# Optimization experiments

Hardware: AMD Instinct MI355X
Metric: run time of the kernel (lower is better)

Reference implementation:

```python
import jax, jax.numpy as jnp
import numpy as np

V, H, L, T, B, S = 32000, 1024, 2, 64, 32, 64


def setup_inputs() -> dict:
    key = jax.random.key(0)
    ks = jax.random.split(key, 10)
    sc = 0.02
    return {
        "tokens": jax.random.randint(ks[0], (T, B), 0, V),
        "h0": jax.random.normal(ks[1], (L, B, H), jnp.float32) * sc,
        "c0": jax.random.normal(ks[2], (L, B, H), jnp.float32) * sc,
        "contexts": jax.random.normal(ks[3], (B, S, H), jnp.float32) * sc,
        "emb": jax.random.normal(ks[4], (V, H), jnp.float32) * sc,
        "W_ih": jax.random.normal(ks[5], (L, 4 * H, H), jnp.float32) * sc,
        "W_hh": jax.random.normal(ks[6], (L, 4 * H, H), jnp.float32) * sc,
        "b_ih": jnp.zeros((L, 4 * H), jnp.float32),
        "b_hh": jnp.zeros((L, 4 * H), jnp.float32),
        "W_in": jax.random.normal(ks[7], (H, H), jnp.float32) * sc,
        "b_in": jnp.zeros((H,), jnp.float32),
        "W_out": jax.random.normal(ks[8], (H, 2 * H), jnp.float32) * sc,
        "b_out": jnp.zeros((H,), jnp.float32),
    }


def _lstm_cell(x, h, c, Wih, Whh, bih, bhh):
    # PyTorch LSTMCell gate order: i, f, g, o
    gates = x @ Wih.T + bih + h @ Whh.T + bhh  # [B, 4H]
    i, f, g, o = jnp.split(gates, 4, axis=-1)
    c1 = jax.nn.sigmoid(f) * c + jax.nn.sigmoid(i) * jnp.tanh(g)
    h1 = jax.nn.sigmoid(o) * jnp.tanh(c1)
    return h1, c1


def reference(tokens, h0, c0, contexts, emb, W_ih, W_hh, b_ih, b_hh,
              W_in, b_in, W_out, b_out):
    # dropout is identity in eval mode
    embs = emb[tokens]  # [T, B, H]
    n_layers = h0.shape[0]

    def step(carry, x):
        h, c = carry
        hs, cs = [], []
        inp = x
        for l in range(n_layers):
            h1, c1 = _lstm_cell(inp, h[l], c[l], W_ih[l], W_hh[l], b_ih[l], b_hh[l])
            inp = h1
            hs.append(h1)
            cs.append(c1)
        # global (Luong general) attention
        gamma = inp @ W_in.T + b_in                      # [B, H]
        scores = jnp.einsum("bsh,bh->bs", contexts, gamma)
        w = jax.nn.softmax(scores, axis=-1)              # [B, S]
        ctx = jnp.einsum("bs,bsh->bh", w, contexts)      # [B, H]
        out = jnp.tanh(jnp.concatenate([ctx, inp], axis=-1) @ W_out.T + b_out)
        return (jnp.stack(hs), jnp.stack(cs)), (out, w)

    (hT, cT), (outputs, attns) = jax.lax.scan(step, (h0, c0), embs)
    return outputs, hT, cT  # outputs: [T, B, H]
```

## Files before the change

### kernel.cpp

```cpp
#include <hip/hip_runtime.h>
#include <hip/hip_bf16.h>

#define HDIM 1024
#define BDIM 32
#define TDIM 64
#define SDIM 64
#define NBLK 256

typedef __attribute__((ext_vector_type(8))) short short8;
typedef __attribute__((ext_vector_type(4))) short s4v;
typedef __attribute__((ext_vector_type(4))) float f32x4;
typedef unsigned short ushort;
typedef unsigned int uint;

__device__ __forceinline__ float sigm(float x){ return 1.f/(1.f+expf(-x)); }
__device__ __forceinline__ ushort f2bf(float x){
  uint u = __float_as_uint(x);
  u = (u + 0x7FFF + ((u>>16)&1)) >> 16;
  return (ushort)u;
}
#define MFMA16(a,b,c) __builtin_amdgcn_mfma_f32_16x16x32_bf16((a),(b),(c),0,0,0)
#define ALD(p)     __hip_atomic_load((p), __ATOMIC_RELAXED, __HIP_MEMORY_SCOPE_AGENT)
#define AST(p,v)   __hip_atomic_store((p),(v), __ATOMIC_RELAXED, __HIP_MEMORY_SCOPE_AGENT)

__device__ __forceinline__ void load8(const char* b, s4v* r){
  asm volatile(
    "global_load_dwordx2 %0, %8, off\n\t"
    "global_load_dwordx2 %1, %8, off offset:128\n\t"
    "global_load_dwordx2 %2, %8, off offset:256\n\t"
    "global_load_dwordx2 %3, %8, off offset:384\n\t"
    "global_load_dwordx2 %4, %8, off offset:2048\n\t"
    "global_load_dwordx2 %5, %8, off offset:2176\n\t"
    "global_load_dwordx2 %6, %8, off offset:2304\n\t"
    "global_load_dwordx2 %7, %8, off offset:2432\n\t"
    : "=&v"(r[0]), "=&v"(r[1]), "=&v"(r[2]), "=&v"(r[3]),
      "=&v"(r[4]), "=&v"(r[5]), "=&v"(r[6]), "=&v"(r[7])
    : "v"(b) : "memory");
}


__global__ void init_state_kernel(const float* __restrict__ h0,
                                  ushort* __restrict__ h0h,
                                  ushort* __restrict__ h1h){
  int i = blockIdx.x*256 + threadIdx.x;
  int l = i >> 15, r = i & 32767;
  int b = r >> 10, h = r & 1023;
  ushort* dst = l ? h1h : h0h;
  dst[(h>>2)*128 + b*4 + (h&3)] = f2bf(h0[i]);
}

__global__ void bar_init_kernel(int* flags){
  for(int i=threadIdx.x; i<1024; i+=256) flags[i] = 0;
}

__global__ void cast_kernel(const float* __restrict__ src, ushort* __restrict__ dst, int n4){
  int i = blockIdx.x*256 + threadIdx.x;
  if(i < n4){
    float4 v = ((const float4*)src)[i];
    ushort4 o; o.x=f2bf(v.x); o.y=f2bf(v.y); o.z=f2bf(v.z); o.w=f2bf(v.w);
    ((ushort4*)dst)[i] = o;
  }
}

__global__ void transpose_ctx_kernel(const float* __restrict__ ctx, ushort* __restrict__ ctxT){
  int b = blockIdx.y;
  int n = blockIdx.x*64 + (threadIdx.x & 63);
  int s0 = (threadIdx.x >> 6) * 16;
  for(int s=s0; s<s0+16; s++){
    float v = ctx[((size_t)b*SDIM + s)*HDIM + n];
    ctxT[((size_t)b*HDIM + n)*SDIM + s] = f2bf(v);
  }
}

__global__ void bias_kernel(const float* __restrict__ b_ih, const float* __restrict__ b_hh,
                            float* __restrict__ bias0, float* __restrict__ bias1){
  int i = blockIdx.x*256 + threadIdx.x;
  bias0[i] = b_ih[i] + b_hh[i];
  bias1[i] = b_ih[4096+i] + b_hh[4096+i];
}

__global__ void embed_kernel(const int* __restrict__ tokens,
                             const float* __restrict__ emb,
                             ushort* __restrict__ Xb){
  int tb = blockIdx.x;
  int tok = tokens[tb];
  const float4* src = (const float4*)(emb + (size_t)tok*HDIM);
  ushort4* dst = (ushort4*)(Xb + (size_t)tb*HDIM);
  float4 v = src[threadIdx.x];
  ushort4 o; o.x=f2bf(v.x); o.y=f2bf(v.y); o.z=f2bf(v.z); o.w=f2bf(v.w);
  dst[threadIdx.x] = o;
}

__global__ __launch_bounds__(256) void gemm_mfma_bt(
    const ushort* __restrict__ A0, const ushort* __restrict__ A1, int lda, int KSPLIT,
    const ushort* __restrict__ B, int ldb,
    const float* __restrict__ bias,
    float* __restrict__ C, int ldc, int K, int act){
  __shared__ ushort As[64][40];
  __shared__ ushort Bs[64][40];
  const int bm = blockIdx.y*64, bn = blockIdx.x*64;
  const int tid = threadIdx.x, w = tid>>6, lane = tid&63;
  const int quad = lane>>4, l16 = lane&15;
  const int mh = (w>>1)*32, nh = (w&1)*32;
  const int arow = tid>>2, aseg = (tid&3)*8;
  f32x4 acc[2][2];
  #pragma unroll
  for(int i=0;i<2;i++)
    #pragma unroll
    for(int j=0;j<2;j++) acc[i][j] = (f32x4){0.f,0.f,0.f,0.f};

  for(int k0=0;k0<K;k0+=32){
    int gk = k0 + aseg;
    const ushort* ap = (gk < KSPLIT) ? (A0 + (size_t)(bm+arow)*lda + gk)
                                     : (A1 + (size_t)(bm+arow)*lda + (gk - KSPLIT));
    *(float4*)&As[arow][aseg] = *(const float4*)ap;
    *(float4*)&Bs[arow][aseg] = *(const float4*)(B + (size_t)(bn+arow)*ldb + k0 + aseg);
    __syncthreads();
    short8 a0 = *(const short8*)&As[mh + l16][quad*8];
    short8 a1 = *(const short8*)&As[mh + 16 + l16][quad*8];
    short8 b0 = *(const short8*)&Bs[nh + l16][quad*8];
    short8 b1 = *(const short8*)&Bs[nh + 16 + l16][quad*8];
    acc[0][0] = MFMA16(a0, b0, acc[0][0]);
    acc[0][1] = MFMA16(a0, b1, acc[0][1]);
    acc[1][0] = MFMA16(a1, b0, acc[1][0]);
    acc[1][1] = MFMA16(a1, b1, acc[1][1]);
    __syncthreads();
  }
  #pragma unroll
  for(int mi=0;mi<2;mi++){
    #pragma unroll
    for(int r=0;r<4;r++){
      int row = bm + mh + mi*16 + quad*4 + r;
      #pragma unroll
      for(int ni=0;ni<2;ni++){
        int col = bn + nh + ni*16 + l16;
        float v = acc[mi][ni][r];
        if(bias) v += bias[col];
        if(act==1) v = tanhf(v);
        if(act==2) ((ushort*)C)[(size_t)row*ldc + col] = f2bf(v);
        else       C[(size_t)row*ldc + col] = v;
      }
    }
  }
}

__global__ __launch_bounds__(256,1) void lstm_skew(
    const ushort* __restrict__ Whh0b,
    const ushort* __restrict__ Wih1b,
    const ushort* __restrict__ Whh1b,
    const float*  __restrict__ G0,
    const float*  __restrict__ bias1c,
    const float*  __restrict__ c0in,
    ushort* __restrict__ h0h,
    ushort* __restrict__ h1h,
    ushort* __restrict__ inp_bf,
    float*  __restrict__ outstate,
    int* __restrict__ flags){
  extern __shared__ char smem[];
  ushort (*W0s)[1032]   = (ushort(*)[1032])smem;
  ushort (*W1s)[2056]   = (ushort(*)[2056])(smem + 33024);
  typedef float gredT[4][32][17];
  gredT* gred0 = (gredT*)(smem + 98816);
  gredT* gred1 = (gredT*)(smem + 116224);
  float (*cloc0)[4]      = (float(*)[4])(smem + 133632);
  float (*cloc1)[4]      = (float(*)[4])(smem + 134144);

  const int tid = threadIdx.x, w = tid>>6, lane = tid&63;
  const int quad = lane>>4, l16 = lane&15;
  const int blk = blockIdx.x;
  const int j0 = blk*4;

  {
    int r = tid>>4, seg = tid&15;
    int wr = (r>>2)*1024 + j0 + (r&3);
    const ushort* s0 = Whh0b + (size_t)wr*1024 + seg*64;
    const ushort* s1 = Wih1b + (size_t)wr*1024 + seg*64;
    const ushort* s2 = Whh1b + (size_t)wr*1024 + seg*64;
    #pragma unroll
    for(int u=0; u<64; u+=8){
      *(short8*)&W0s[r][seg*64+u]       = *(const short8*)(s0+u);
      *(short8*)&W1s[r][seg*64+u]       = *(const short8*)(s1+u);
      *(short8*)&W1s[r][1024+seg*64+u]  = *(const short8*)(s2+u);
    }
  }
  if(tid < 128){
    int b = tid>>2, jj = tid&3;
    cloc0[b][jj] = c0in[b*1024 + j0 + jj];
    cloc1[b][jj] = c0in[32768 + b*1024 + j0 + jj];
  }
  float2 pbI={0,0}, pbF={0,0}, pbG={0,0}, pbO={0,0};
  if(tid >= 64 && tid < 128){
    const float* br = bias1c + j0 + ((tid-64)&1)*2;
    pbI = *(const float2*)(br);
    pbF = *(const float2*)(br+1024);
    pbG = *(const float2*)(br+2048);
    pbO = *(const float2*)(br+3072);
  }
  __syncthreads();

  for(int p=0; p<=TDIM; p++){
    const int par = p&1;
    const ushort* h0p = h0h + (size_t)p*32768;
    ushort*       h0n = h0h + (size_t)(p+1)*32768;
    const ushort* h1m = h1h + (size_t)(p>0?p-1:0)*32768;
    ushort*       h1c = h1h + (size_t)p*32768;

    float2 pgI={0,0}, pgF={0,0}, pgG={0,0}, pgO={0,0};
    if(p < TDIM && tid < 64){
      const float* g0r = G0 + (size_t)(p*32+(tid>>1))*4096 + j0 + (tid&1)*2;
      pgI = *(const float2*)(g0r);
      pgF = *(const float2*)(g0r+1024);
      pgG = *(const float2*)(g0r+2048);
      pgO = *(const float2*)(g0r+3072);
    }

    s4v r0[32]; s4v r1[64];
    if(p < TDIM){
      const char* b0 = (const char*)h0p + w*16384 + quad*512 + l16*8;
      load8(b0,        r0);
      load8(b0+4096,   r0+8);
      load8(b0+8192,   r0+16);
      load8(b0+12288,  r0+24);
    }
    if(p > 0){
      const char* b1 = (const char*)((w<2)?h0p:h1m) + (w&1)*32768 + quad*512 + l16*8;
      #pragma unroll
      for(int i=0;i<8;i++) load8(b1 + i*4096, r1 + i*8);
    }
    asm volatile("s_waitcnt vmcnt(0)" ::: "memory");
    __builtin_amdgcn_sched_barrier(0);

    if(p < TDIM){
      f32x4 acc0 = {0,0,0,0}, acc1 = {0,0,0,0};
      #pragma unroll
      for(int kc=0;kc<8;kc++){
        short8 af0 = __builtin_shufflevector(r0[kc*4+0], r0[kc*4+2], 0,1,2,3,4,5,6,7);
        short8 af1 = __builtin_shufflevector(r0[kc*4+1], r0[kc*4+3], 0,1,2,3,4,5,6,7);
        short8 bfrag = *(const short8*)&W0s[l16][w*256 + kc*32 + quad*8];
        acc0 = MFMA16(af0, bfrag, acc0);
        acc1 = MFMA16(af1, bfrag, acc1);
      }
      #pragma unroll
      for(int r=0;r<4;r++){
        gred0[par][w][quad*4+r][l16]    = acc0[r];
        gred0[par][w][16+quad*4+r][l16] = acc1[r];
      }
    }
    if(p > 0){
      f32x4 acc0 = {0,0,0,0}, acc1 = {0,0,0,0};
      #pragma unroll
      for(int kc=0;kc<16;kc++){
        short8 af0 = __builtin_shufflevector(r1[kc*4+0], r1[kc*4+2], 0,1,2,3,4,5,6,7);
        short8 af1 = __builtin_shufflevector(r1[kc*4+1], r1[kc*4+3], 0,1,2,3,4,5,6,7);
        short8 bfrag = *(const short8*)&W1s[l16][w*512 + kc*32 + quad*8];
        acc0 = MFMA16(af0, bfrag, acc0);
        acc1 = MFMA16(af1, bfrag, acc1);
      }
      #pragma unroll
      for(int r=0;r<4;r++){
        gred1[par][w][quad*4+r][l16]    = acc0[r];
        gred1[par][w][16+quad*4+r][l16] = acc1[r];
      }
    }
    __syncthreads();
    if(p < TDIM && tid < 64){
      int b = tid>>1, j2 = (tid&1)*2;
      ushort hv[2];
      #pragma unroll
      for(int u=0;u<2;u++){
        int jj = j2+u;
        float gi = u ? pgI.y : pgI.x;
        float gf = u ? pgF.y : pgF.x;
        float gg = u ? pgG.y : pgG.x;
        float go = u ? pgO.y : pgO.x;
        #pragma unroll
        for(int ww=0;ww<4;ww++){
          gi += gred0[par][ww][b][jj];    gf += gred0[par][ww][b][4+jj];
          gg += gred0[par][ww][b][8+jj];  go += gred0[par][ww][b][12+jj];
        }
        float c = cloc0[b][jj];
        float c1 = sigm(gf)*c + sigm(gi)*tanhf(gg);
        float h1 = sigm(go)*tanhf(c1);
        cloc0[b][jj] = c1;
        hv[u] = f2bf(h1);
        if(p==TDIM-1){
          outstate[b*1024 + j0 + jj] = h1;
          outstate[65536 + b*1024 + j0 + jj] = c1;
        }
      }
      uint pk = (uint)hv[0] | ((uint)hv[1] << 16);
      AST((uint*)(h0n + blk*128 + b*4 + j2), pk);
    }
    if(p > 0 && tid >= 64 && tid < 128){
      int ct = tid-64;
      int b = ct>>1, j2 = (ct&1)*2;
      ushort hv[2];
      #pragma unroll
      for(int u=0;u<2;u++){
        int jj = j2+u;
        float gi = u ? pbI.y : pbI.x;
        float gf = u ? pbF.y : pbF.x;
        float gg = u ? pbG.y : pbG.x;
        float go = u ? pbO.y : pbO.x;
        #pragma unroll
        for(int ww=0;ww<4;ww++){
          gi += gred1[par][ww][b][jj];    gf += gred1[par][ww][b][4+jj];
          gg += gred1[par][ww][b][8+jj];  go += gred1[par][ww][b][12+jj];
        }
        float c = cloc1[b][jj];
        float c1 = sigm(gf)*c + sigm(gi)*tanhf(gg);
        float h1 = sigm(go)*tanhf(c1);
        cloc1[b][jj] = c1;
        hv[u] = f2bf(h1);
        inp_bf[(size_t)((p-1)*32+b)*1024 + j0 + jj] = hv[u];
        if(p==TDIM){
          outstate[32768 + b*1024 + j0 + jj] = h1;
          outstate[98304 + b*1024 + j0 + jj] = c1;
        }
      }
      uint pk = (uint)hv[0] | ((uint)hv[1] << 16);
      AST((uint*)(h1c + blk*128 + b*4 + j2), pk);
    }
    if(p == TDIM) break;

    const int target = p+1;
    if(tid < 128){
      asm volatile("s_waitcnt vmcnt(0)" ::: "memory");
      if((tid&63)==0) AST(&flags[blk*2 + w], target);
    }
    if(blk==0 && tid < 64){
      while(true){
        int mn = 0x7fffffff;
        #pragma unroll
        for(int q=0;q<8;q++){ int v = ALD(&flags[tid + q*64]); mn = min(mn, v); }
        if(__all(mn >= target)) break;
        __builtin_amdgcn_s_sleep(1);
      }
      if(tid < 16) AST(&flags[512 + tid*32], target);
    }
    while(ALD(&flags[512 + (blk>>4)*32]) < target) __builtin_amdgcn_s_sleep(1);
  }
}

__global__ __launch_bounds__(256) void attn_mfma(
    const ushort* __restrict__ gamma_bf,
    const ushort* __restrict__ ctxb,
    const ushort* __restrict__ ctxT,
    ushort* __restrict__ ctx_out){
  const int b = blockIdx.y, t0 = blockIdx.x*16;
  const int tid = threadIdx.x, w = tid>>6, lane = tid&63;
  const int quad = lane>>4, l16 = lane&15;
  __shared__ float S[16][68];
  __shared__ ushort Pb[16][72];
  {
    f32x4 acc = {0,0,0,0};
    const ushort* arow = gamma_bf + ((size_t)(t0+l16)*32 + b)*1024;
    const ushort* brow = ctxb + ((size_t)b*SDIM + w*16 + l16)*1024;
    #pragma unroll 8
    for(int kc=0;kc<32;kc++){
      short8 af = *(const short8*)(arow + kc*32 + quad*8);
      short8 bf = *(const short8*)(brow + kc*32 + quad*8);
      acc = MFMA16(af, bf, acc);
    }
    #pragma unroll
    for(int r=0;r<4;r++) S[quad*4+r][w*16+l16] = acc[r];
  }
  __syncthreads();
  if(tid < 16){
    float mx = -1e30f;
    for(int s=0;s<SDIM;s++) mx = fmaxf(mx, S[tid][s]);
    float sum = 0.f;
    for(int s=0;s<SDIM;s++) sum += expf(S[tid][s]-mx);
    float inv = 1.f/sum;
    for(int s=0;s<SDIM;s++) Pb[tid][s] = f2bf(expf(S[tid][s]-mx)*inv);
  }
  __syncthreads();
  const ushort* bbase = ctxT + ((size_t)b*HDIM + w*256)*SDIM;
  for(int nt=0; nt<16; nt++){
    f32x4 acc = {0,0,0,0};
    #pragma unroll
    for(int kc=0;kc<2;kc++){
      short8 af = *(const short8*)&Pb[l16][kc*32 + quad*8];
      short8 bf = *(const short8*)(bbase + (size_t)(nt*16+l16)*SDIM + kc*32 + quad*8);
      acc = MFMA16(af, bf, acc);
    }
    int n = w*256 + nt*16 + l16;
    #pragma unroll
    for(int r=0;r<4;r++){
      int t = t0 + quad*4 + r;
      ctx_out[((size_t)t*32 + b)*1024 + n] = f2bf(acc[r]);
    }
  }
}

extern "C" void kernel_launch(void* const* d_in, const int* in_sizes, int n_in,
                              void* d_out, int out_size, void* d_ws, size_t ws_size,
                              hipStream_t stream){
  const int*   tokens   = (const int*)  d_in[0];
  const float* h0       = (const float*)d_in[1];
  const float* c0       = (const float*)d_in[2];
  const float* contexts = (const float*)d_in[3];
  const float* emb      = (const float*)d_in[4];
  const float* W_ih     = (const float*)d_in[5];
  const float* W_hh     = (const float*)d_in[6];
  const float* b_ih     = (const float*)d_in[7];
  const float* b_hh     = (const float*)d_in[8];
  const float* W_in     = (const float*)d_in[9];
  const float* b_in     = (const float*)d_in[10];
  const float* W_out    = (const float*)d_in[11];
  const float* b_out    = (const float*)d_in[12];

  float* out = (float*)d_out;
  const int TB = TDIM*BDIM;

  char* wp = (char*)d_ws;
  float* G0      = (float*)wp;  wp += (size_t)TB*4*HDIM*4;
  float* bias0c  = (float*)wp;  wp += 4096*4;
  float* bias1c  = (float*)wp;  wp += 4096*4;
  int*   flags   = (int*)wp;    wp += 4096;
  ushort* X_bf   = (ushort*)wp; wp += (size_t)TB*HDIM*2;
  ushort* Wih0b  = (ushort*)wp; wp += (size_t)4*HDIM*HDIM*2;
  ushort* Whh0b  = (ushort*)wp; wp += (size_t)4*HDIM*HDIM*2;
  ushort* Wih1b  = (ushort*)wp; wp += (size_t)4*HDIM*HDIM*2;
  ushort* Whh1b  = (ushort*)wp; wp += (size_t)4*HDIM*HDIM*2;
  ushort* Winb   = (ushort*)wp; wp += (size_t)HDIM*HDIM*2;
  ushort* Woutb  = (ushort*)wp; wp += (size_t)HDIM*2*HDIM*2;
  ushort* inp_bf = (ushort*)wp; wp += (size_t)TB*HDIM*2;
  ushort* h0hist = (ushort*)wp; wp += (size_t)(TDIM+1)*BDIM*HDIM*2;
  ushort* h1hist = (ushort*)wp; wp += (size_t)(TDIM+1)*BDIM*HDIM*2;
  ushort* ctxb_bf= (ushort*)wp; wp += (size_t)BDIM*SDIM*HDIM*2;
  ushort* ctxT_bf= (ushort*)wp; wp += (size_t)BDIM*SDIM*HDIM*2;
  ushort* gammaB = (ushort*)G0;
  ushort* ctx_bf = X_bf;

  init_state_kernel<<<256,256,0,stream>>>(h0, h0hist, h1hist);
  bar_init_kernel<<<1,256,0,stream>>>(flags);
  cast_kernel<<<4096,256,0,stream>>>(W_ih,                       Wih0b, 4*HDIM*HDIM/4);
  cast_kernel<<<4096,256,0,stream>>>(W_hh,                       Whh0b, 4*HDIM*HDIM/4);
  cast_kernel<<<4096,256,0,stream>>>(W_ih + (size_t)4*HDIM*HDIM, Wih1b, 4*HDIM*HDIM/4);
  cast_kernel<<<4096,256,0,stream>>>(W_hh + (size_t)4*HDIM*HDIM, Whh1b, 4*HDIM*HDIM/4);
  cast_kernel<<<1024,256,0,stream>>>(W_in,  Winb,  HDIM*HDIM/4);
  cast_kernel<<<2048,256,0,stream>>>(W_out, Woutb, HDIM*2*HDIM/4);
  cast_kernel<<<2048,256,0,stream>>>(contexts, ctxb_bf, BDIM*SDIM*HDIM/4);
  transpose_ctx_kernel<<<dim3(16,32),256,0,stream>>>(contexts, ctxT_bf);
  bias_kernel<<<16,256,0,stream>>>(b_ih, b_hh, bias0c, bias1c);
  embed_kernel<<<TB,256,0,stream>>>(tokens, emb, X_bf);

  gemm_mfma_bt<<<dim3(4*HDIM/64, TB/64),256,0,stream>>>(
      X_bf, X_bf, HDIM, HDIM, Wih0b, HDIM, bias0c, G0, 4*HDIM, HDIM, 0);

  lstm_skew<<<NBLK,256,134656,stream>>>(
      Whh0b, Wih1b, Whh1b, G0, bias1c, c0,
      h0hist, h1hist, inp_bf, out + (size_t)TB*HDIM, flags);

  gemm_mfma_bt<<<dim3(HDIM/64, TB/64),256,0,stream>>>(
      inp_bf, inp_bf, HDIM, HDIM, Winb, HDIM, b_in, (float*)gammaB, HDIM, HDIM, 2);

  attn_mfma<<<dim3(4,32),256,0,stream>>>(gammaB, ctxb_bf, ctxT_bf, ctx_bf);

  gemm_mfma_bt<<<dim3(HDIM/64, TB/64),256,0,stream>>>(
      ctx_bf, inp_bf, HDIM, HDIM, Woutb, 2*HDIM, b_out, out, HDIM, 2*HDIM, 1);
}
```

Before: 890.4 us.

## Skew layer-1 by two steps to overlap its input GEMM with the barrier

The persistent LSTM kernel now runs layer 1 two steps behind layer 0, so the layer-1 input product (from the previous step's layer-0 h) can be computed before the grid-wide barrier wait. Only the recurrent loads happen after the barrier, and the barrier wait moves to the top of each iteration with split vmcnt waits. Separately, seven weight and context cast launches are merged into one fused cast kernel to cut launch overhead. This adds one extra pipeline step, one more h0 history slot, and more complex indexing that must stay correct.

New measurement: 820.1 us. -7.9%, faster.

```diff
diff --git a/kernel.cpp b/kernel.cpp
--- a/kernel.cpp
+++ b/kernel.cpp
@@ -10,6 +10,7 @@
 typedef __attribute__((ext_vector_type(8))) short short8;
 typedef __attribute__((ext_vector_type(4))) short s4v;
 typedef __attribute__((ext_vector_type(4))) float f32x4;
+typedef __attribute__((ext_vector_type(2))) float f32x2;
 typedef unsigned short ushort;
 typedef unsigned int uint;
 
@@ -53,13 +54,28 @@
   for(int i=threadIdx.x; i<1024; i+=256) flags[i] = 0;
 }
 
-__global__ void cast_kernel(const float* __restrict__ src, ushort* __restrict__ dst, int n4){
-  int i = blockIdx.x*256 + threadIdx.x;
-  if(i < n4){
-    float4 v = ((const float4*)src)[i];
-    ushort4 o; o.x=f2bf(v.x); o.y=f2bf(v.y); o.z=f2bf(v.z); o.w=f2bf(v.w);
-    ((ushort4*)dst)[i] = o;
-  }
+__global__ void fused_cast_kernel(
+    const float* __restrict__ W_ih, const float* __restrict__ W_hh,
+    const float* __restrict__ W_in, const float* __restrict__ W_out,
+    const float* __restrict__ ctx,
+    ushort* __restrict__ Wih0b, ushort* __restrict__ Whh0b,
+    ushort* __restrict__ Wih1b, ushort* __restrict__ Whh1b,
+    ushort* __restrict__ Winb,  ushort* __restrict__ Woutb,
+    ushort* __restrict__ ctxb){
+  long i = (long)blockIdx.x*256 + threadIdx.x;
+  const float* src; ushort* dst; long off;
+  if(i < 2097152){
+    if(i < 1048576){ src=W_ih;          dst=Wih0b; off=i; }
+    else           { src=W_hh;          dst=Whh0b; off=i-1048576; }
+  } else if(i < 4194304){
+    if(i < 3145728){ src=W_ih+4194304;  dst=Wih1b; off=i-2097152; }
+    else           { src=W_hh+4194304;  dst=Whh1b; off=i-3145728; }
+  } else if(i < 4456448){ src=W_in;     dst=Winb;  off=i-4194304; }
+  else if(i < 4980736){   src=W_out;    dst=Woutb; off=i-4456448; }
+  else {                  src=ctx;      dst=ctxb;  off=i-4980736; }
+  float4 v = ((const float4*)src)[off];
+  ushort4 o; o.x=f2bf(v.x); o.y=f2bf(v.y); o.z=f2bf(v.z); o.w=f2bf(v.w);
+  ((ushort4*)dst)[off] = o;
 }
 
 __global__ void transpose_ctx_kernel(const float* __restrict__ ctx, ushort* __restrict__ ctxT){
@@ -198,72 +214,124 @@
   }
   __syncthreads();
 
-  for(int p=0; p<=TDIM; p++){
+  for(int p=0; p<=TDIM+1; p++){
     const int par = p&1;
-    const ushort* h0p = h0h + (size_t)p*32768;
-    ushort*       h0n = h0h + (size_t)(p+1)*32768;
-    const ushort* h1m = h1h + (size_t)(p>0?p-1:0)*32768;
-    ushort*       h1c = h1h + (size_t)p*32768;
-
-    float2 pgI={0,0}, pgF={0,0}, pgG={0,0}, pgO={0,0};
-    if(p < TDIM && tid < 64){
+    const bool doL0 = (p < TDIM);
+    const bool doL1 = (p >= 2);
+    const ushort* h0p    = h0h + (size_t)p*32768;
+    ushort*       h0n    = h0h + (size_t)(p+1)*32768;
+    const ushort* h0prev = h0h + (size_t)(p>=1?p-1:0)*32768;
+    const ushort* h1m    = h1h + (size_t)(p>=2?p-2:0)*32768;
+    ushort*       h1c    = h1h + (size_t)(p>=1?p-1:0)*32768;
+
+    f32x4 accA0 = {0,0,0,0}, accA1 = {0,0,0,0};
+
+    f32x2 pgI={0,0}, pgF={0,0}, pgG={0,0}, pgO={0,0};
+    if(doL0 && tid < 64){
       const float* g0r = G0 + (size_t)(p*32+(tid>>1))*4096 + j0 + (tid&1)*2;
-      pgI = *(const float2*)(g0r);
-      pgF = *(const float2*)(g0r+1024);
-      pgG = *(const float2*)(g0r+2048);
-      pgO = *(const float2*)(g0r+3072);
-    }
-
-    s4v r0[32]; s4v r1[64];
-    if(p < TDIM){
-      const char* b0 = (const char*)h0p + w*16384 + quad*512 + l16*8;
-      load8(b0,        r0);
-      load8(b0+4096,   r0+8);
-      load8(b0+8192,   r0+16);
-      load8(b0+12288,  r0+24);
-    }
-    if(p > 0){
-      const char* b1 = (const char*)((w<2)?h0p:h1m) + (w&1)*32768 + quad*512 + l16*8;
-      #pragma unroll
-      for(int i=0;i<8;i++) load8(b1 + i*4096, r1 + i*8);
-    }
-    asm volatile("s_waitcnt vmcnt(0)" ::: "memory");
-    __builtin_amdgcn_sched_barrier(0);
-
-    if(p < TDIM){
-      f32x4 acc0 = {0,0,0,0}, acc1 = {0,0,0,0};
-      #pragma unroll
-      for(int kc=0;kc<8;kc++){
-        short8 af0 = __builtin_shufflevector(r0[kc*4+0], r0[kc*4+2], 0,1,2,3,4,5,6,7);
-        short8 af1 = __builtin_shufflevector(r0[kc*4+1], r0[kc*4+3], 0,1,2,3,4,5,6,7);
-        short8 bfrag = *(const short8*)&W0s[l16][w*256 + kc*32 + quad*8];
-        acc0 = MFMA16(af0, bfrag, acc0);
-        acc1 = MFMA16(af1, bfrag, acc1);
-      }
-      #pragma unroll
-      for(int r=0;r<4;r++){
-        gred0[par][w][quad*4+r][l16]    = acc0[r];
-        gred0[par][w][16+quad*4+r][l16] = acc1[r];
-      }
-    }
-    if(p > 0){
-      f32x4 acc0 = {0,0,0,0}, acc1 = {0,0,0,0};
-      #pragma unroll
-      for(int kc=0;kc<16;kc++){
-        short8 af0 = __builtin_shufflevector(r1[kc*4+0], r1[kc*4+2], 0,1,2,3,4,5,6,7);
-        short8 af1 = __builtin_shufflevector(r1[kc*4+1], r1[kc*4+3], 0,1,2,3,4,5,6,7);
-        short8 bfrag = *(const short8*)&W1s[l16][w*512 + kc*32 + quad*8];
-        acc0 = MFMA16(af0, bfrag, acc0);
-        acc1 = MFMA16(af1, bfrag, acc1);
-      }
-      #pragma unroll
-      for(int r=0;r<4;r++){
-        gred1[par][w][quad*4+r][l16]    = acc0[r];
-        gred1[par][w][16+quad*4+r][l16] = acc1[r];
+      asm volatile(
+        "global_load_dwordx2 %0, %4, off\n\t"
+        "global_load_dwordx2 %1, %5, off\n\t"
+        "global_load_dwordx2 %2, %6, off\n\t"
+        "global_load_dwordx2 %3, %7, off"
+        : "=&v"(pgI), "=&v"(pgF), "=&v"(pgG), "=&v"(pgO)
+        : "v"(g0r), "v"(g0r+1024), "v"(g0r+2048), "v"(g0r+3072)
+        : "memory");
+    }
+    {
+      s4v ra[32];
+      if(doL1){
+        const char* ba = (const char*)h0prev + w*16384 + quad*512 + l16*8;
+        load8(ba,       ra);
+        load8(ba+4096,  ra+8);
+        load8(ba+8192,  ra+16);
+        load8(ba+12288, ra+24);
+      }
+      asm volatile("s_waitcnt vmcnt(0)" ::: "memory");
+      __builtin_amdgcn_sched_barrier(0);
+      if(doL1){
+        #pragma unroll
+        for(int kc=0;kc<8;kc++){
+          short8 af0 = __builtin_shufflevector(ra[kc*4+0], ra[kc*4+2], 0,1,2,3,4,5,6,7);
+          short8 af1 = __builtin_shufflevector(ra[kc*4+1], ra[kc*4+3], 0,1,2,3,4,5,6,7);
+          short8 bfrag = *(const short8*)&W1s[l16][w*256 + kc*32 + quad*8];
+          accA0 = MFMA16(af0, bfrag, accA0);
+          accA1 = MFMA16(af1, bfrag, accA1);
+        }
+      }
+    }
+
+    if(p >= 1){
+      const int target = p;
+      if(blk==0 && tid<64){
+        while(true){
+          int mn = 0x7fffffff;
+          #pragma unroll
+          for(int q=0;q<8;q++){ int v = ALD(&flags[tid + q*64]); mn = min(mn, v); }
+          if(__all(mn >= target)) break;
+          __builtin_amdgcn_s_sleep(1);
+        }
+        if(tid < 16) AST(&flags[512 + tid*32], target);
+      }
+      while(ALD(&flags[512 + (blk>>4)*32]) < target) __builtin_amdgcn_s_sleep(1);
+    }
+
+    {
+      s4v rb[32], rc[32];
+      if(doL0){
+        const char* bb = (const char*)h0p + w*16384 + quad*512 + l16*8;
+        load8(bb,       rb);
+        load8(bb+4096,  rb+8);
+        load8(bb+8192,  rb+16);
+        load8(bb+12288, rb+24);
+      }
+      if(doL1){
+        const char* bc = (const char*)h1m + w*16384 + quad*512 + l16*8;
+        load8(bc,       rc);
+        load8(bc+4096,  rc+8);
+        load8(bc+8192,  rc+16);
+        load8(bc+12288, rc+24);
+      }
+      if(doL0){
+        if(doL1) asm volatile("s_waitcnt vmcnt(32)" ::: "memory");
+        else     asm volatile("s_waitcnt vmcnt(0)"  ::: "memory");
+        __builtin_amdgcn_sched_barrier(0);
+        f32x4 acc0 = {0,0,0,0}, acc1 = {0,0,0,0};
+        #pragma unroll
+        for(int kc=0;kc<8;kc++){
+          short8 af0 = __builtin_shufflevector(rb[kc*4+0], rb[kc*4+2], 0,1,2,3,4,5,6,7);
+          short8 af1 = __builtin_shufflevector(rb[kc*4+1], rb[kc*4+3], 0,1,2,3,4,5,6,7);
+          short8 bfrag = *(const short8*)&W0s[l16][w*256 + kc*32 + quad*8];
+          acc0 = MFMA16(af0, bfrag, acc0);
+          acc1 = MFMA16(af1, bfrag, acc1);
+        }
+        #pragma unroll
+        for(int r=0;r<4;r++){
+          gred0[par][w][quad*4+r][l16]    = acc0[r];
+          gred0[par][w][16+quad*4+r][l16] = acc1[r];
+        }
+      }
+      if(doL1){
+        asm volatile("s_waitcnt vmcnt(0)" ::: "memory");
+        __builtin_amdgcn_sched_barrier(0);
+        #pragma unroll
+        for(int kc=0;kc<8;kc++){
+          short8 af0 = __builtin_shufflevector(rc[kc*4+0], rc[kc*4+2], 0,1,2,3,4,5,6,7);
+          short8 af1 = __builtin_shufflevector(rc[kc*4+1], rc[kc*4+3], 0,1,2,3,4,5,6,7);
+          short8 bfrag = *(const short8*)&W1s[l16][1024 + w*256 + kc*32 + quad*8];
+          accA0 = MFMA16(af0, bfrag, accA0);
+          accA1 = MFMA16(af1, bfrag, accA1);
+        }
+        #pragma unroll
+        for(int r=0;r<4;r++){
+          gred1[par][w][quad*4+r][l16]    = accA0[r];
+          gred1[par][w][16+quad*4+r][l16] = accA1[r];
+        }
       }
     }
     __syncthreads();
-    if(p < TDIM && tid < 64){
+
+    if(doL0 && tid < 64){
       int b = tid>>1, j2 = (tid&1)*2;
       ushort hv[2];
       #pragma unroll
@@ -291,7 +359,7 @@
       uint pk = (uint)hv[0] | ((uint)hv[1] << 16);
       AST((uint*)(h0n + blk*128 + b*4 + j2), pk);
     }
-    if(p > 0 && tid >= 64 && tid < 128){
+    if(doL1 && tid >= 64 && tid < 128){
       int ct = tid-64;
       int b = ct>>1, j2 = (ct&1)*2;
       ushort hv[2];
@@ -312,8 +380,8 @@
         float h1 = sigm(go)*tanhf(c1);
         cloc1[b][jj] = c1;
         hv[u] = f2bf(h1);
-        inp_bf[(size_t)((p-1)*32+b)*1024 + j0 + jj] = hv[u];
-        if(p==TDIM){
+        inp_bf[(size_t)((p-2)*32+b)*1024 + j0 + jj] = hv[u];
+        if(p==TDIM+1){
           outstate[32768 + b*1024 + j0 + jj] = h1;
           outstate[98304 + b*1024 + j0 + jj] = c1;
         }
@@ -321,24 +389,12 @@
       uint pk = (uint)hv[0] | ((uint)hv[1] << 16);
       AST((uint*)(h1c + blk*128 + b*4 + j2), pk);
     }
-    if(p == TDIM) break;
-
-    const int target = p+1;
+    if(p == TDIM+1) break;
+
     if(tid < 128){
       asm volatile("s_waitcnt vmcnt(0)" ::: "memory");
-      if((tid&63)==0) AST(&flags[blk*2 + w], target);
-    }
-    if(blk==0 && tid < 64){
-      while(true){
-        int mn = 0x7fffffff;
-        #pragma unroll
-        for(int q=0;q<8;q++){ int v = ALD(&flags[tid + q*64]); mn = min(mn, v); }
-        if(__all(mn >= target)) break;
-        __builtin_amdgcn_s_sleep(1);
-      }
-      if(tid < 16) AST(&flags[512 + tid*32], target);
-    }
-    while(ALD(&flags[512 + (blk>>4)*32]) < target) __builtin_amdgcn_s_sleep(1);
+      if((tid&63)==0) AST(&flags[blk*2 + w], p+1);
+    }
   }
 }
 
@@ -426,7 +482,7 @@
   ushort* Winb   = (ushort*)wp; wp += (size_t)HDIM*HDIM*2;
   ushort* Woutb  = (ushort*)wp; wp += (size_t)HDIM*2*HDIM*2;
   ushort* inp_bf = (ushort*)wp; wp += (size_t)TB*HDIM*2;
-  ushort* h0hist = (ushort*)wp; wp += (size_t)(TDIM+1)*BDIM*HDIM*2;
+  ushort* h0hist = (ushort*)wp; wp += (size_t)(TDIM+2)*BDIM*HDIM*2;
   ushort* h1hist = (ushort*)wp; wp += (size_t)(TDIM+1)*BDIM*HDIM*2;
   ushort* ctxb_bf= (ushort*)wp; wp += (size_t)BDIM*SDIM*HDIM*2;
   ushort* ctxT_bf= (ushort*)wp; wp += (size_t)BDIM*SDIM*HDIM*2;
@@ -435,13 +491,9 @@
 
   init_state_kernel<<<256,256,0,stream>>>(h0, h0hist, h1hist);
   bar_init_kernel<<<1,256,0,stream>>>(flags);
-  cast_kernel<<<4096,256,0,stream>>>(W_ih,                       Wih0b, 4*HDIM*HDIM/4);
-  cast_kernel<<<4096,256,0,stream>>>(W_hh,                       Whh0b, 4*HDIM*HDIM/4);
-  cast_kernel<<<4096,256,0,stream>>>(W_ih + (size_t)4*HDIM*HDIM, Wih1b, 4*HDIM*HDIM/4);
-  cast_kernel<<<4096,256,0,stream>>>(W_hh + (size_t)4*HDIM*HDIM, Whh1b, 4*HDIM*HDIM/4);
-  cast_kernel<<<1024,256,0,stream>>>(W_in,  Winb,  HDIM*HDIM/4);
-  cast_kernel<<<2048,256,0,stream>>>(W_out, Woutb, HDIM*2*HDIM/4);
-  cast_kernel<<<2048,256,0,stream>>>(contexts, ctxb_bf, BDIM*SDIM*HDIM/4);
+  fused_cast_kernel<<<21504,256,0,stream>>>(
+      W_ih, W_hh, W_in, W_out, contexts,
+      Wih0b, Whh0b, Wih1b, Whh1b, Winb, Woutb, ctxb_bf);
   transpose_ctx_kernel<<<dim3(16,32),256,0,stream>>>(contexts, ctxT_bf);
   bias_kernel<<<16,256,0,stream>>>(b_ih, b_hh, bias0c, bias1c);
   embed_kernel<<<TB,256,0,stream>>>(tokens, emb, X_bf);
```
